# Optimization experiments

Hardware: AMD Instinct MI355X
Metric: run time of the kernel (lower is better)

Reference implementation:

```python
import jax, jax.numpy as jnp
import numpy as np

B, S, D, H = 4, 2048, 512, 8
HD = D // H  # head_dim = 64


def setup_inputs() -> dict:
    key = jax.random.key(0)
    ks = jax.random.split(key, 16)
    sd = 1.0 / np.sqrt(D)
    def lin(ka, kb):
        W = jax.random.uniform(ka, (D, D), jnp.float32, -sd, sd)
        b = jax.random.uniform(kb, (D,), jnp.float32, -sd, sd)
        return W, b
    Wq, bq = lin(ks[0], ks[1])
    Wk, bk = lin(ks[2], ks[3])
    Wv, bv = lin(ks[4], ks[5])
    Wo, bo = lin(ks[6], ks[7])
    Ws, bs = lin(ks[8], ks[9])
    Wsh, bsh = lin(ks[10], ks[11])
    mod1_feat = jax.random.normal(ks[12], (B, S, D), jnp.float32)
    mod2_feat = jax.random.normal(ks[13], (B, S, D), jnp.float32)
    return {"mod1_feat": mod1_feat, "mod2_feat": mod2_feat,
            "Wq": Wq, "bq": bq, "Wk": Wk, "bk": bk, "Wv": Wv, "bv": bv,
            "Wo": Wo, "bo": bo, "Ws": Ws, "bs": bs, "Wsh": Wsh, "bsh": bsh}


def _heads(x):
    # [B, S, D] -> [B, H, S, HD]
    b, s, _ = x.shape
    return x.reshape(b, s, H, HD).transpose(0, 2, 1, 3)


def reference(mod1_feat, mod2_feat, Wq, bq, Wk, bk, Wv, bv, Wo, bo, Ws, bs, Wsh, bsh):
    Q = _heads(mod1_feat @ Wq + bq)
    K = _heads(mod2_feat @ Wk + bk)
    V = _heads(mod2_feat @ Wv + bv)
    scale = _heads(mod2_feat @ Ws + bs)
    shift = _heads(mod2_feat @ Wsh + bsh)
    K = K * scale + shift
    V = V * scale + shift
    scores = jnp.einsum('bhqd,bhkd->bhqk', Q, K) / jnp.sqrt(jnp.float32(HD))
    attn = jax.nn.softmax(scores, axis=-1)
    out = jnp.einsum('bhqk,bhkd->bhqd', attn, V)  # [B, H, S, HD]
    out = out.transpose(0, 2, 1, 3).reshape(mod1_feat.shape[0], -1, H * HD)
    return out @ Wo + bo
```

## Files before the change

kernel.cpp:

```cpp
#include <hip/hip_runtime.h>
#include <hip/hip_bf16.h>
#include <cstdint>
#include <cstddef>

typedef __bf16 bf16_t;
typedef __bf16 bf16x8 __attribute__((ext_vector_type(8)));
typedef __bf16 bf16x4 __attribute__((ext_vector_type(4)));
typedef float f32x4 __attribute__((ext_vector_type(4)));

#define DEVINL static __device__ __forceinline__

constexpr int B_ = 4, S_ = 2048, D_ = 512, H_ = 8, HD_ = 64;
constexpr int M_ = B_ * S_;
constexpr int NIN = 14;

DEVINL bf16x8 load8g(const bf16_t* p) { return *reinterpret_cast<const bf16x8*>(p); }

DEVINL int swcol(int col, int row) {
  return (col & ~63) | ((((col >> 3) ^ row) & 7) << 3) | (col & 7);
}

DEVINL void gl2lds(const bf16_t* g, bf16_t* l) {
  __builtin_amdgcn_global_load_lds(
      (const __attribute__((address_space(1))) void*)g,
      (__attribute__((address_space(3))) void*)l, 16, 0, 0);
}

DEVINL void stage16(bf16_t* dst, const void* src, size_t off, bool f32) {
  if (f32) {
    const float* p = (const float*)src + off;
    bf16x8 v0, v1;
#pragma unroll
    for (int j = 0; j < 8; ++j) { v0[j] = (bf16_t)p[j]; v1[j] = (bf16_t)p[8 + j]; }
    *reinterpret_cast<bf16x8*>(dst)     = v0;
    *reinterpret_cast<bf16x8*>(dst + 8) = v1;
  } else {
    const bf16_t* p = (const bf16_t*)src + off;
    *reinterpret_cast<bf16x8*>(dst)     = load8g(p);
    *reinterpret_cast<bf16x8*>(dst + 8) = load8g(p + 8);
  }
}

DEVINL float readf(const void* p, size_t i, bool f32) {
  return f32 ? ((const float*)p)[i] : (float)((const bf16_t*)p)[i];
}

struct DetectArgs { const uint16_t* p[NIN]; int n[NIN]; int* flags; };

__global__ __launch_bounds__(64) void detect_kernel(DetectArgs a) {
  const int z = blockIdx.x;
  const uint16_t* p = a.p[z];
  const int n = a.n[z];
  const int t = threadIdx.x;
  int cnt = 0;
  for (int i = t; i < n; i += 64) {
    const int e = (p[i] >> 7) & 0xFF;
    cnt += (e >= 200);
  }
#pragma unroll
  for (int off = 32; off > 0; off >>= 1) cnt += __shfl_down(cnt, off, 64);
  if (t == 0) a.flags[z] = (cnt > 16) ? 1 : 0;
}

struct CvtArgs { const void* src[2]; bf16_t* dst[2]; int idx[2]; const int* flags; };

__global__ __launch_bounds__(256) void cvt_kernel(CvtArgs a) {
  const int z = blockIdx.y;
  const bool f32 = a.flags[a.idx[z]] != 0;
  const size_t i = ((size_t)blockIdx.x * 256 + threadIdx.x) * 8;
  const int row = (int)(i >> 9);
  const int col = (int)(i & 511);
  bf16_t* dst = a.dst[z] + (size_t)row * 512 + swcol(col, row);
  if (f32) {
    const float* p = (const float*)a.src[z] + i;
    bf16x8 v;
#pragma unroll
    for (int j = 0; j < 8; ++j) v[j] = (bf16_t)p[j];
    *reinterpret_cast<bf16x8*>(dst) = v;
  } else {
    *reinterpret_cast<bf16x8*>(dst) = load8g((const bf16_t*)a.src[z] + i);
  }
}

struct TransArgs { const void* src[6]; int srcIdx[6]; bf16_t* dst[6]; const int* flags; };

__global__ __launch_bounds__(256) void transpose_kernel(TransArgs a) {
  __shared__ bf16_t tile[64][80];
  const int w = blockIdx.z;
  const void* src = a.src[w];
  const bool f32 = a.flags[a.srcIdx[w]] != 0;
  bf16_t* dst = a.dst[w];
  const int k0 = blockIdx.x * 64, n0 = blockIdx.y * 64;
  const int t = threadIdx.x;
  const int r = t >> 2, c0 = (t & 3) * 16;
  stage16(&tile[r][c0], src, (size_t)(k0 + r) * 512 + n0 + c0, f32);
  __syncthreads();
  const int orow = n0 + r;
  bf16_t* o = dst + (size_t)orow * 512;
#pragma unroll
  for (int half = 0; half < 2; ++half) {
    bf16x8 ov;
#pragma unroll
    for (int j = 0; j < 8; ++j) ov[j] = tile[c0 + half * 8 + j][r];
    *reinterpret_cast<bf16x8*>(o + swcol(k0 + c0 + half * 8, orow)) = ov;
  }
}

struct GemmBatch {
  const bf16_t* A[3];
  const bf16_t* Bt[3];
  const void* bias[3]; int bIdx[3];
  void* C[3];          int cIdx[3];
  const int* flags;
};

__global__ __launch_bounds__(256) void gemm_bt_kernel(GemmBatch args) {
  constexpr int K = 512, N = 512;
  __shared__ bf16_t As[2][128][64];
  __shared__ bf16_t Bs[2][64][64];
  const int z = blockIdx.z;
  const bf16_t* Ag  = args.A[z];
  const bf16_t* Btg = args.Bt[z];
  const void* biag  = args.bias[z];
  void* Cg          = args.C[z];
  const bool bf32 = args.bIdx[z] >= 0 && args.flags[args.bIdx[z]];
  const bool cf32 = args.cIdx[z] >= 0 && args.flags[args.cIdx[z]];
  const int m0 = blockIdx.x * 128, n0 = blockIdx.y * 64;
  const int t = threadIdx.x, lane = t & 63, wave = t >> 6;
  const int l16 = lane & 15, quad = lane >> 4;
  const int wm = wave * 32;
  const int lr = lane >> 3, lc = (lane & 7) * 8;

  auto stage = [&](int buf, int k0) {
#pragma unroll
    for (int s = 0; s < 4; ++s) {
      const int r = wm + s * 8;
      gl2lds(Ag + (size_t)(m0 + r + lr) * K + k0 + lc, &As[buf][r][0]);
    }
#pragma unroll
    for (int s = 0; s < 2; ++s) {
      const int r = wave * 16 + s * 8;
      gl2lds(Btg + (size_t)(n0 + r + lr) * K + k0 + lc, &Bs[buf][r][0]);
    }
  };

  f32x4 acc[2][4] = {};
  stage(0, 0);

  for (int kt = 0; kt < K / 64; ++kt) {
    const int cur = kt & 1;
    __syncthreads();
    if (kt + 1 < K / 64) stage(1 - cur, (kt + 1) * 64);
#pragma unroll
    for (int ks = 0; ks < 2; ++ks) {
      const int sw = swcol(ks * 32 + quad * 8, l16);
      bf16x8 af[2], bfr[4];
#pragma unroll
      for (int i = 0; i < 2; ++i)
        af[i] = *reinterpret_cast<const bf16x8*>(&As[cur][wm + i * 16 + l16][sw]);
#pragma unroll
      for (int j = 0; j < 4; ++j)
        bfr[j] = *reinterpret_cast<const bf16x8*>(&Bs[cur][j * 16 + l16][sw]);
#pragma unroll
      for (int i = 0; i < 2; ++i)
#pragma unroll
        for (int j = 0; j < 4; ++j)
          acc[i][j] = __builtin_amdgcn_mfma_f32_16x16x32_bf16(af[i], bfr[j], acc[i][j], 0, 0, 0);
    }
  }
#pragma unroll
  for (int j = 0; j < 4; ++j) {
    const int col = n0 + j * 16 + l16;
    const float bv = readf(biag, col, bf32);
#pragma unroll
    for (int i = 0; i < 2; ++i) {
      const int rowb = m0 + wm + i * 16 + quad * 4;
#pragma unroll
      for (int r = 0; r < 4; ++r) {
        const size_t idx = (size_t)(rowb + r) * N + col;
        const float v = acc[i][j][r] + bv;
        if (cf32) ((float*)Cg)[idx] = v;
        else      ((bf16_t*)Cg)[idx] = (bf16_t)v;
      }
    }
  }
}

struct GemmModArgs {
  const bf16_t* A;
  const bf16_t* Bt[2];
  const void* bias[2]; int bIdx[2];
  const bf16_t* Sc;
  const bf16_t* Sh;
  bf16_t* Kmod;
  bf16_t* VtT;
  const int* flags;
};

__global__ __launch_bounds__(256) void gemm_mod_kernel(GemmModArgs args) {
  constexpr int K = 512;
  __shared__ bf16_t As[2][128][64];
  __shared__ bf16_t Bs[2][64][64];
  const int z = blockIdx.z;
  const bf16_t* Ag  = args.A;
  const bf16_t* Btg = args.Bt[z];
  const void* biag  = args.bias[z];
  const bool bf32 = args.bIdx[z] >= 0 && args.flags[args.bIdx[z]];
  const int m0 = blockIdx.x * 128, n0 = blockIdx.y * 64;
  const int t = threadIdx.x, lane = t & 63, wave = t >> 6;
  const int l16 = lane & 15, quad = lane >> 4;
  const int wm = wave * 32;
  const int lr = lane >> 3, lc = (lane & 7) * 8;

  auto stage = [&](int buf, int k0) {
#pragma unroll
    for (int s = 0; s < 4; ++s) {
      const int r = wm + s * 8;
      gl2lds(Ag + (size_t)(m0 + r + lr) * K + k0 + lc, &As[buf][r][0]);
    }
#pragma unroll
    for (int s = 0; s < 2; ++s) {
      const int r = wave * 16 + s * 8;
      gl2lds(Btg + (size_t)(n0 + r + lr) * K + k0 + lc, &Bs[buf][r][0]);
    }
  };

  f32x4 acc[2][4] = {};
  stage(0, 0);

  for (int kt = 0; kt < K / 64; ++kt) {
    const int cur = kt & 1;
    __syncthreads();
    if (kt + 1 < K / 64) stage(1 - cur, (kt + 1) * 64);
#pragma unroll
    for (int ks = 0; ks < 2; ++ks) {
      const int sw = swcol(ks * 32 + quad * 8, l16);
      bf16x8 af[2], bfr[4];
#pragma unroll
      for (int i = 0; i < 2; ++i)
        af[i] = *reinterpret_cast<const bf16x8*>(&As[cur][wm + i * 16 + l16][sw]);
#pragma unroll
      for (int j = 0; j < 4; ++j)
        bfr[j] = *reinterpret_cast<const bf16x8*>(&Bs[cur][j * 16 + l16][sw]);
#pragma unroll
      for (int i = 0; i < 2; ++i)
#pragma unroll
        for (int j = 0; j < 4; ++j)
          acc[i][j] = __builtin_amdgcn_mfma_f32_16x16x32_bf16(af[i], bfr[j], acc[i][j], 0, 0, 0);
    }
  }
#pragma unroll
  for (int j = 0; j < 4; ++j) {
    const int col = n0 + j * 16 + l16;
    const float bv = readf(biag, col, bf32);
#pragma unroll
    for (int i = 0; i < 2; ++i) {
      const int rowb = m0 + wm + i * 16 + quad * 4;
      if (z == 0) {
#pragma unroll
        for (int r = 0; r < 4; ++r) {
          const int row = rowb + r;
          const size_t idx = (size_t)row * 512 + col;
          const float sc = (float)args.Sc[idx], sh = (float)args.Sh[idx];
          args.Kmod[(size_t)row * 512 + swcol(col, row)] = (bf16_t)fmaf(acc[i][j][r] + bv, sc, sh);
        }
      } else {
        bf16x4 pack;
#pragma unroll
        for (int r = 0; r < 4; ++r) {
          const size_t idx = (size_t)(rowb + r) * 512 + col;
          const float sc = (float)args.Sc[idx], sh = (float)args.Sh[idx];
          pack[r] = (bf16_t)fmaf(acc[i][j][r] + bv, sc, sh);
        }
        const int bb = rowb >> 11;
        const int ss = rowb & 2047;
        const int hh = col >> 6, dd = col & 63;
        *reinterpret_cast<bf16x4*>(
            args.VtT + (((size_t)(bb * H_ + hh)) * HD_ + dd) * S_ + swcol(ss, dd)) = pack;
      }
    }
  }
}

__global__ __launch_bounds__(256) void attn_kernel(const bf16_t* Q, const bf16_t* Kb,
                                                   const bf16_t* Vt, bf16_t* O) {
  __shared__ bf16_t Ks[2][64][64];
  __shared__ bf16_t Vs[2][64][64];
  __shared__ bf16_t Pw[4][32][72];
  const int i = blockIdx.x;
  const int xcd = i & 7, g = i >> 3;
  const int slice = xcd * 4 + (g & 3);
  const int qt = g >> 2;
  const int b = slice >> 3, h = slice & 7;
  const int t = threadIdx.x, wave = t >> 6, lane = t & 63;
  const int l16 = lane & 15, quad = lane >> 4;
  const int q0 = qt * 128 + wave * 32;
  const int lr = lane >> 3, lc = (lane & 7) * 8;
  const int sw0 = swcol(quad * 8, l16), sw1 = swcol(32 + quad * 8, l16);

  bf16x8 ones;
#pragma unroll
  for (int j = 0; j < 8; ++j) ones[j] = (bf16_t)1.0f;

  bf16x8 qf[2][2];
#pragma unroll
  for (int qs = 0; qs < 2; ++qs) {
    const size_t qrow = ((size_t)b * S_ + q0 + qs * 16 + l16) * D_ + h * HD_;
    qf[qs][0] = load8g(Q + qrow + quad * 8);
    qf[qs][1] = load8g(Q + qrow + 32 + quad * 8);
  }

  f32x4 oacc[2][4] = {};
  f32x4 lacc[2] = {};

  const size_t kbase = (size_t)b * S_ * D_ + h * HD_;
  const size_t vbase = ((size_t)(b * H_ + h)) * HD_ * S_;

  auto stage = [&](int buf, int k0) {
#pragma unroll
    for (int s = 0; s < 2; ++s) {
      const int r = wave * 16 + s * 8;
      gl2lds(Kb + kbase + (size_t)(k0 + r + lr) * D_ + lc, &Ks[buf][r][0]);
      gl2lds(Vt + vbase + (size_t)(r + lr) * S_ + k0 + lc, &Vs[buf][r][0]);
    }
  };

  stage(0, 0);

  for (int kt = 0; kt < S_ / 64; ++kt) {
    const int cur = kt & 1;
    __syncthreads();
    if (kt + 1 < S_ / 64) stage(1 - cur, (kt + 1) * 64);
    f32x4 sacc[4][2] = {};
#pragma unroll
    for (int c = 0; c < 2; ++c) {
      const int sw = c ? sw1 : sw0;
      bf16x8 kf[4];
#pragma unroll
      for (int j = 0; j < 4; ++j)
        kf[j] = *reinterpret_cast<const bf16x8*>(&Ks[cur][j * 16 + l16][sw]);
#pragma unroll
      for (int j = 0; j < 4; ++j)
#pragma unroll
        for (int qs = 0; qs < 2; ++qs)
          sacc[j][qs] = __builtin_amdgcn_mfma_f32_16x16x32_bf16(kf[j], qf[qs][c], sacc[j][qs], 0, 0, 0);
    }
#pragma unroll
    for (int j = 0; j < 4; ++j)
#pragma unroll
      for (int qs = 0; qs < 2; ++qs) {
        bf16x4 pack;
#pragma unroll
        for (int r = 0; r < 4; ++r)
          pack[r] = (bf16_t)__expf(fminf(sacc[j][qs][r] * 0.125f, 40.0f));
        *reinterpret_cast<bf16x4*>(&Pw[wave][qs * 16 + l16][j * 16 + quad * 4]) = pack;
      }
#pragma unroll
    for (int c = 0; c < 2; ++c) {
      const int sw = c ? sw1 : sw0;
      bf16x8 bp[2];
#pragma unroll
      for (int qs = 0; qs < 2; ++qs)
        bp[qs] = *reinterpret_cast<const bf16x8*>(&Pw[wave][qs * 16 + l16][c * 32 + quad * 8]);
      bf16x8 vf[4];
#pragma unroll
      for (int dj = 0; dj < 4; ++dj)
        vf[dj] = *reinterpret_cast<const bf16x8*>(&Vs[cur][dj * 16 + l16][sw]);
#pragma unroll
      for (int qs = 0; qs < 2; ++qs) {
#pragma unroll
        for (int dj = 0; dj < 4; ++dj)
          oacc[qs][dj] = __builtin_amdgcn_mfma_f32_16x16x32_bf16(vf[dj], bp[qs], oacc[qs][dj], 0, 0, 0);
        lacc[qs] = __builtin_amdgcn_mfma_f32_16x16x32_bf16(ones, bp[qs], lacc[qs], 0, 0, 0);
      }
    }
  }
#pragma unroll
  for (int qs = 0; qs < 2; ++qs) {
    const float linv = 1.0f / fmaxf(lacc[qs][0], 1e-30f);
    const int q = q0 + qs * 16 + l16;
    const size_t orow = ((size_t)b * S_ + q) * D_ + h * HD_;
#pragma unroll
    for (int dj = 0; dj < 4; ++dj) {
      bf16x4 pack;
#pragma unroll
      for (int r = 0; r < 4; ++r) pack[r] = (bf16_t)(oacc[qs][dj][r] * linv);
      *reinterpret_cast<bf16x4*>(&O[orow + swcol(dj * 16 + quad * 4, q)]) = pack;
    }
  }
}

extern "C" void kernel_launch(void* const* d_in, const int* in_sizes, int n_in,
                              void* d_out, int out_size, void* d_ws, size_t ws_size,
                              hipStream_t stream) {
  (void)n_in; (void)out_size; (void)ws_size;

  char* ws = (char*)d_ws;
  auto alloc = [&](size_t bytes) -> char* {
    char* p = ws; ws += (bytes + 255) & ~(size_t)255; return p;
  };
  int* flags = (int*)alloc(64 * sizeof(int));
  const size_t wbytes = (size_t)512 * 512 * sizeof(bf16_t);
  const size_t fbytes = (size_t)M_ * D_ * sizeof(bf16_t);
  bf16_t* wt    = (bf16_t*)alloc(6 * wbytes);
  bf16_t* m1b   = (bf16_t*)alloc(fbytes);
  bf16_t* m2b   = (bf16_t*)alloc(fbytes);
  bf16_t* q_buf = (bf16_t*)alloc(fbytes);
  bf16_t* stmp  = (bf16_t*)alloc(fbytes);
  bf16_t* shtmp = (bf16_t*)alloc(fbytes);
  bf16_t* kmod  = (bf16_t*)alloc(fbytes);
  bf16_t* vtb    = m1b;
  bf16_t* attn_b = stmp;

  bf16_t* wtq  = wt + 0 * 512 * 512;
  bf16_t* wtk  = wt + 1 * 512 * 512;
  bf16_t* wtv  = wt + 2 * 512 * 512;
  bf16_t* wts  = wt + 3 * 512 * 512;
  bf16_t* wtsh = wt + 4 * 512 * 512;
  bf16_t* wto  = wt + 5 * 512 * 512;

  DetectArgs da;
  for (int i = 0; i < NIN; ++i) {
    da.p[i] = (const uint16_t*)d_in[i];
    da.n[i] = in_sizes[i] < 2048 ? in_sizes[i] : 2048;
  }
  da.flags = flags;
  hipLaunchKernelGGL(detect_kernel, dim3(NIN), dim3(64), 0, stream, da);

  CvtArgs ca;
  ca.src[0] = d_in[0]; ca.dst[0] = m1b; ca.idx[0] = 0;
  ca.src[1] = d_in[1]; ca.dst[1] = m2b; ca.idx[1] = 1;
  ca.flags = flags;
  hipLaunchKernelGGL(cvt_kernel, dim3(M_ * D_ / 2048, 2), dim3(256), 0, stream, ca);

  TransArgs ta;
  const int widx[6] = {2, 4, 6, 10, 12, 8};
  bf16_t* wdst[6] = {wtq, wtk, wtv, wts, wtsh, wto};
  for (int i = 0; i < 6; ++i) { ta.src[i] = d_in[widx[i]]; ta.srcIdx[i] = widx[i]; ta.dst[i] = wdst[i]; }
  ta.flags = flags;
  hipLaunchKernelGGL(transpose_kernel, dim3(8, 8, 6), dim3(256), 0, stream, ta);

  GemmBatch g1;
  g1.A[0] = m1b; g1.A[1] = m2b; g1.A[2] = m2b;
  g1.Bt[0] = wtq; g1.Bt[1] = wts; g1.Bt[2] = wtsh;
  g1.bias[0] = d_in[3];  g1.bIdx[0] = 3;
  g1.bias[1] = d_in[11]; g1.bIdx[1] = 11;
  g1.bias[2] = d_in[13]; g1.bIdx[2] = 13;
  g1.C[0] = q_buf; g1.cIdx[0] = -1;
  g1.C[1] = stmp;  g1.cIdx[1] = -1;
  g1.C[2] = shtmp; g1.cIdx[2] = -1;
  g1.flags = flags;
  hipLaunchKernelGGL(gemm_bt_kernel, dim3(M_ / 128, 8, 3), dim3(256), 0, stream, g1);

  GemmModArgs gm;
  gm.A = m2b;
  gm.Bt[0] = wtk; gm.Bt[1] = wtv;
  gm.bias[0] = d_in[5]; gm.bIdx[0] = 5;
  gm.bias[1] = d_in[7]; gm.bIdx[1] = 7;
  gm.Sc = stmp; gm.Sh = shtmp;
  gm.Kmod = kmod; gm.VtT = vtb;
  gm.flags = flags;
  hipLaunchKernelGGL(gemm_mod_kernel, dim3(M_ / 128, 8, 2), dim3(256), 0, stream, gm);

  hipLaunchKernelGGL(attn_kernel, dim3(512), dim3(256), 0, stream,
                     q_buf, kmod, vtb, attn_b);

  GemmBatch g2;
  for (int i = 0; i < 3; ++i) {
    g2.A[i] = attn_b;
    g2.Bt[i] = wto;
    g2.bias[i] = d_in[9]; g2.bIdx[i] = 9;
    g2.C[i] = d_out; g2.cIdx[i] = 0;
  }
  g2.flags = flags;
  hipLaunchKernelGGL(gemm_bt_kernel, dim3(M_ / 128, 8, 1), dim3(256), 0, stream, g2);
}
```

Baseline: 233.9 us.

## Keep softmax probabilities in registers by permuting K row layout

K rows are stored with a permuted swizzle so that the MFMA output layout of the score tile lines up with the B-operand layout the PV MFMA expects. The exponentiated scores can then be packed straight into registers, which removes the per-wave LDS buffer and its write/read round trip. The exponential now uses exp2 with a prescaled constant. This relies on the K producer and the attention consumer agreeing on the new swizzle, so any mismatch between them would silently corrupt results.

```diff
diff --git a/kernel.cpp b/kernel.cpp
--- a/kernel.cpp
+++ b/kernel.cpp
@@ -18,6 +18,11 @@
 
 DEVINL int swcol(int col, int row) {
   return (col & ~63) | ((((col >> 3) ^ row) & 7) << 3) | (col & 7);
+}
+
+DEVINL int pK(int row) { return (row & 3) | (((row >> 3) & 1) << 2); }
+DEVINL int swcolK(int col, int row) {
+  return (col & ~63) | ((((col >> 3) ^ pK(row)) & 7) << 3) | (col & 7);
 }
 
 DEVINL void gl2lds(const bf16_t* g, bf16_t* l) {
@@ -262,7 +267,7 @@
           const int row = rowb + r;
           const size_t idx = (size_t)row * 512 + col;
           const float sc = (float)args.Sc[idx], sh = (float)args.Sh[idx];
-          args.Kmod[(size_t)row * 512 + swcol(col, row)] = (bf16_t)fmaf(acc[i][j][r] + bv, sc, sh);
+          args.Kmod[(size_t)row * 512 + swcolK(col, row)] = (bf16_t)fmaf(acc[i][j][r] + bv, sc, sh);
         }
       } else {
         bf16x4 pack;
@@ -286,7 +291,6 @@
                                                    const bf16_t* Vt, bf16_t* O) {
   __shared__ bf16_t Ks[2][64][64];
   __shared__ bf16_t Vs[2][64][64];
-  __shared__ bf16_t Pw[4][32][72];
   const int i = blockIdx.x;
   const int xcd = i & 7, g = i >> 3;
   const int slice = xcd * 4 + (g & 3);
@@ -296,7 +300,6 @@
   const int l16 = lane & 15, quad = lane >> 4;
   const int q0 = qt * 128 + wave * 32;
   const int lr = lane >> 3, lc = (lane & 7) * 8;
-  const int sw0 = swcol(quad * 8, l16), sw1 = swcol(32 + quad * 8, l16);
 
   bf16x8 ones;
 #pragma unroll
@@ -316,6 +319,17 @@
   const size_t kbase = (size_t)b * S_ * D_ + h * HD_;
   const size_t vbase = ((size_t)(b * H_ + h)) * HD_ * S_;
 
+  const int rbase = ((l16 >> 2) << 3) | (l16 & 3);
+  int koff[2][4];
+#pragma unroll
+  for (int j = 0; j < 4; ++j) {
+    const int rho = rbase + (j >> 1) * 32 + (j & 1) * 4;
+#pragma unroll
+    for (int dc = 0; dc < 2; ++dc)
+      koff[dc][j] = rho * 64 + swcolK(dc * 32 + quad * 8, rho);
+  }
+  const int voff[2] = { swcol(quad * 8, l16), swcol(32 + quad * 8, l16) };
+
   auto stage = [&](int buf, int k0) {
 #pragma unroll
     for (int s = 0; s < 2; ++s) {
@@ -326,52 +340,45 @@
   };
 
   stage(0, 0);
+
+  constexpr float CE = 0.18033688011112042f;
 
   for (int kt = 0; kt < S_ / 64; ++kt) {
     const int cur = kt & 1;
     __syncthreads();
     if (kt + 1 < S_ / 64) stage(1 - cur, (kt + 1) * 64);
     f32x4 sacc[4][2] = {};
-#pragma unroll
-    for (int c = 0; c < 2; ++c) {
-      const int sw = c ? sw1 : sw0;
+    const bf16_t* ksbase = &Ks[cur][0][0];
+#pragma unroll
+    for (int dc = 0; dc < 2; ++dc) {
       bf16x8 kf[4];
 #pragma unroll
       for (int j = 0; j < 4; ++j)
-        kf[j] = *reinterpret_cast<const bf16x8*>(&Ks[cur][j * 16 + l16][sw]);
+        kf[j] = *reinterpret_cast<const bf16x8*>(ksbase + koff[dc][j]);
 #pragma unroll
       for (int j = 0; j < 4; ++j)
 #pragma unroll
         for (int qs = 0; qs < 2; ++qs)
-          sacc[j][qs] = __builtin_amdgcn_mfma_f32_16x16x32_bf16(kf[j], qf[qs][c], sacc[j][qs], 0, 0, 0);
-    }
-#pragma unroll
-    for (int j = 0; j < 4; ++j)
+          sacc[j][qs] = __builtin_amdgcn_mfma_f32_16x16x32_bf16(kf[j], qf[qs][dc], sacc[j][qs], 0, 0, 0);
+    }
+#pragma unroll
+    for (int kc = 0; kc < 2; ++kc) {
+      bf16x8 vf[4];
+#pragma unroll
+      for (int dj = 0; dj < 4; ++dj)
+        vf[dj] = *reinterpret_cast<const bf16x8*>(&Vs[cur][dj * 16 + l16][voff[kc]]);
 #pragma unroll
       for (int qs = 0; qs < 2; ++qs) {
-        bf16x4 pack;
-#pragma unroll
-        for (int r = 0; r < 4; ++r)
-          pack[r] = (bf16_t)__expf(fminf(sacc[j][qs][r] * 0.125f, 40.0f));
-        *reinterpret_cast<bf16x4*>(&Pw[wave][qs * 16 + l16][j * 16 + quad * 4]) = pack;
-      }
-#pragma unroll
-    for (int c = 0; c < 2; ++c) {
-      const int sw = c ? sw1 : sw0;
-      bf16x8 bp[2];
-#pragma unroll
-      for (int qs = 0; qs < 2; ++qs)
-        bp[qs] = *reinterpret_cast<const bf16x8*>(&Pw[wave][qs * 16 + l16][c * 32 + quad * 8]);
-      bf16x8 vf[4];
-#pragma unroll
-      for (int dj = 0; dj < 4; ++dj)
-        vf[dj] = *reinterpret_cast<const bf16x8*>(&Vs[cur][dj * 16 + l16][sw]);
-#pragma unroll
-      for (int qs = 0; qs < 2; ++qs) {
+        bf16x8 bp;
+#pragma unroll
+        for (int r = 0; r < 4; ++r) {
+          bp[r]     = (bf16_t)__builtin_amdgcn_exp2f(fminf(sacc[kc * 2][qs][r]     * CE, 57.5f));
+          bp[4 + r] = (bf16_t)__builtin_amdgcn_exp2f(fminf(sacc[kc * 2 + 1][qs][r] * CE, 57.5f));
+        }
 #pragma unroll
         for (int dj = 0; dj < 4; ++dj)
-          oacc[qs][dj] = __builtin_amdgcn_mfma_f32_16x16x32_bf16(vf[dj], bp[qs], oacc[qs][dj], 0, 0, 0);
-        lacc[qs] = __builtin_amdgcn_mfma_f32_16x16x32_bf16(ones, bp[qs], lacc[qs], 0, 0, 0);
+          oacc[qs][dj] = __builtin_amdgcn_mfma_f32_16x16x32_bf16(vf[dj], bp, oacc[qs][dj], 0, 0, 0);
+        lacc[qs] = __builtin_amdgcn_mfma_f32_16x16x32_bf16(ones, bp, lacc[qs], 0, 0, 0);
       }
     }
   }
```

New measurement: 229.2 us. -2.0%, faster.
